# Kernel tuning notes

Hardware: AMD Instinct MI355X
Metric: run time of the kernel (lower is better)

The kernel has to match this reference:

```python
import jax, jax.numpy as jnp
import numpy as np


def setup_inputs() -> dict:
    key = jax.random.key(0)
    k1, k2 = jax.random.split(key)
    B, Lc, Lm, D = 8, 2048, 2048, 128
    context = jax.random.normal(k1, (B, Lc, D), dtype=jnp.float32)
    main = jax.random.normal(k2, (B, Lm, D), dtype=jnp.float32)
    return {"context": context, "main": main}


def reference(context, main):
    # weights[b,c,m] = sum_d context[b,c,d] * main[b,m,d]   (Keras dot axes=[2,2])
    weights = jnp.einsum("bcd,bmd->bcm", context, main)
    # K.softmax default axis=-1: normalize over the main-length axis m
    weights = jax.nn.softmax(weights, axis=-1)
    # dot([weights, context], axes=1): contract axis 1 (c) of both -> (B, Lm, D)
    weighted = jnp.einsum("bcm,bcd->bmd", weights, context)
    return main - weighted
```

## Files before the change

kernel.cpp:

```cpp
#include <hip/hip_runtime.h>


#define BATCH 8
#define L_SEQ 2048
#define DD 128
#define SHIFT 40.0f
#define LDA 136
#define TLD 136

typedef __attribute__((ext_vector_type(8))) short bf16x8;
typedef __attribute__((ext_vector_type(4))) float f32x4;
typedef __attribute__((ext_vector_type(16))) float f32x16;
typedef __attribute__((ext_vector_type(4))) unsigned int uint4v;

__device__ __forceinline__ short f2bf(float f) {
    unsigned u = __builtin_bit_cast(unsigned, f);
    return (short)((u + 0x8000u) >> 16);
}

template <int NT>
__device__ __forceinline__ void stage_tile(short* __restrict__ dst,
                                           const float* __restrict__ src,
                                           int nelts, int t) {
    for (int base = 0; base < nelts; base += NT * 8) {
        int flat = base + t * 8;
        const float4* p = (const float4*)(src + flat);
        float4 v0 = p[0];
        float4 v1 = p[1];
        bf16x8 s;
        s[0] = f2bf(v0.x); s[1] = f2bf(v0.y); s[2] = f2bf(v0.z); s[3] = f2bf(v0.w);
        s[4] = f2bf(v1.x); s[5] = f2bf(v1.y); s[6] = f2bf(v1.z); s[7] = f2bf(v1.w);
        int row = flat >> 7;
        int col = flat & 127;
        *(bf16x8*)&dst[row * LDA + col] = s;
    }
}

__global__ __launch_bounds__(256) void zero_kernel(float* __restrict__ p, int n) {
    int i = blockIdx.x * 256 + threadIdx.x;
    if (i < n) p[i] = 0.0f;
}


__global__ __launch_bounds__(256) void convert_kernel(const float* __restrict__ ctx,
                                                      const float* __restrict__ mn,
                                                      short* __restrict__ Cf,
                                                      short* __restrict__ Mf,
                                                      short* __restrict__ Ctf) {
    __shared__ short Ts[32 * TLD];

    int bid = blockIdx.x;
    int tsel = bid & 1;
    int b = (bid >> 1) & 7;
    int rg = bid >> 4;
    int t = threadIdx.x;

    const float* src = (tsel ? mn : ctx) + ((size_t)(b * L_SEQ + rg * 32)) * DD;

    #pragma unroll
    for (int i = 0; i < 2; ++i) {
        int flat = i * 2048 + t * 8;
        int r = flat >> 7;
        int d = flat & 127;
        const float4* p = (const float4*)(src + flat);
        float4 v0 = p[0];
        float4 v1 = p[1];
        bf16x8 s;
        s[0] = f2bf(v0.x); s[1] = f2bf(v0.y); s[2] = f2bf(v0.z); s[3] = f2bf(v0.w);
        s[4] = f2bf(v1.x); s[5] = f2bf(v1.y); s[6] = f2bf(v1.z); s[7] = f2bf(v1.w);
        *(bf16x8*)&Ts[r * TLD + d] = s;
    }
    __syncthreads();

    if (tsel == 0) {
        int cs = rg >> 2;
        int ch = rg & 3;
        size_t cfb = (size_t)(((b * 16 + cs) * 4 + ch) * 8) * 512;
        #pragma unroll
        for (int i = 0; i < 2; ++i) {
            int slot = i * 256 + t;
            int ks = slot >> 6;
            int l2 = slot & 63;
            int la = l2 & 31;
            int hi = l2 >> 5;
            bf16x8 v = *(const bf16x8*)&Ts[la * TLD + (ks * 2 + hi) * 8];
            *(bf16x8*)&Cf[cfb + (size_t)ks * 512 + l2 * 8] = v;
        }
        size_t ctb = (size_t)((((b * 16 + cs) * 4 + ch) * 4) * 2) * 512;
        #pragma unroll
        for (int i = 0; i < 2; ++i) {
            int slot = i * 256 + t;
            int recl = slot >> 6;
            int l2 = slot & 63;
            int dg = recl >> 1;
            int ks2 = recl & 1;
            int la = l2 & 31;
            int hi = l2 >> 5;
            int d = dg * 32 + la;
            int c0 = (ks2 * 2 + hi) * 8;
            bf16x8 v;
            #pragma unroll
            for (int j = 0; j < 8; ++j) v[j] = Ts[(c0 + j) * TLD + d];
            *(bf16x8*)&Ctf[ctb + (size_t)recl * 512 + l2 * 8] = v;
        }
    } else {
        size_t mfb = (size_t)((b * 64 + rg) * 8) * 512;
        #pragma unroll
        for (int i = 0; i < 2; ++i) {
            int slot = i * 256 + t;
            int ks = slot >> 6;
            int l2 = slot & 63;
            int la = l2 & 31;
            int hi = l2 >> 5;
            bf16x8 v = *(const bf16x8*)&Ts[la * TLD + (ks * 2 + hi) * 8];
            *(bf16x8*)&Mf[mfb + (size_t)ks * 512 + l2 * 8] = v;
        }
    }
}

__global__ __launch_bounds__(512) void stats_kernel(const short* __restrict__ Cf,
                                                    const short* __restrict__ Mf,
                                                    float* __restrict__ invLg) {
    __shared__ float red[8][2][32];

    int bid = blockIdx.x;
    int b = bid & 7;
    int ct2 = bid >> 3;
    int t = threadIdx.x;
    int w = t >> 6;
    int l = t & 63;
    int la = l & 31;

    bf16x8 cf[2][8];
    #pragma unroll
    for (int j = 0; j < 2; ++j) {
        int ct = ct2 * 2 + j;
        const short* cfp = Cf + (size_t)(((b * 16 + (ct >> 2)) * 4 + (ct & 3)) * 8) * 512 + l * 8;
        #pragma unroll
        for (int ks = 0; ks < 8; ++ks)
            cf[j][ks] = *(const bf16x8*)&cfp[(size_t)ks * 512];
    }

    float lacc0 = 0.0f, lacc1 = 0.0f;
    for (int i = 0; i < 8; ++i) {
        int mw = w * 8 + i;
        const short* mfp = Mf + (size_t)((b * 64 + mw) * 8) * 512 + l * 8;
        f32x16 s0, s1;
        #pragma unroll
        for (int r = 0; r < 16; ++r) { s0[r] = 0.0f; s1[r] = 0.0f; }
        #pragma unroll
        for (int ks = 0; ks < 8; ++ks) {
            bf16x8 av = *(const bf16x8*)&mfp[(size_t)ks * 512];
            s0 = __builtin_amdgcn_mfma_f32_32x32x16_bf16(av, cf[0][ks], s0, 0, 0, 0);
            s1 = __builtin_amdgcn_mfma_f32_32x32x16_bf16(av, cf[1][ks], s1, 0, 0, 0);
        }
        #pragma unroll
        for (int r = 0; r < 16; ++r) {
            lacc0 += __expf(s0[r] - SHIFT);
            lacc1 += __expf(s1[r] - SHIFT);
        }
    }

    lacc0 += __shfl_xor(lacc0, 32);
    lacc1 += __shfl_xor(lacc1, 32);
    if (l < 32) { red[w][0][la] = lacc0; red[w][1][la] = lacc1; }
    __syncthreads();
    if (t < 64) {
        int j = t >> 5;
        int c = t & 31;
        float L = 0.0f;
        #pragma unroll
        for (int ww = 0; ww < 8; ++ww) L += red[ww][j][c];
        invLg[(size_t)b * L_SEQ + ct2 * 64 + j * 32 + c] = 1.0f / L;
    }
}

__global__ __launch_bounds__(256, 2) void attend_fused(const short* __restrict__ Cf,
                                                       const short* __restrict__ Mf,
                                                       const short* __restrict__ Ctf,
                                                       const float* __restrict__ invLg,
                                                       const float* __restrict__ mn,
                                                       float* __restrict__ out) {
    __shared__ float red[4][4096];

    int bid = blockIdx.x;
    int b = bid & 7;
    int mtile = bid >> 3;
    int t = threadIdx.x;
    int w = t >> 6;
    int l = t & 63;
    int la = l & 31;
    int hi = l >> 5;
    int ch = w;

    bf16x8 mf[8];
    {
        const short* mfp = Mf + (size_t)((b * 64 + mtile) * 8) * 512 + l * 8;
        #pragma unroll
        for (int ks = 0; ks < 8; ++ks)
            mf[ks] = *(const bf16x8*)&mfp[(size_t)ks * 512];
    }

    f32x16 o[4];
    #pragma unroll
    for (int dg = 0; dg < 4; ++dg)
        #pragma unroll
        for (int r = 0; r < 16; ++r) o[dg][r] = 0.0f;

    const float* ilbase = invLg + (size_t)b * L_SEQ + ch * 32 + hi * 4;

    for (int cs = 0; cs < 16; ++cs) {
        const short* cfp = Cf + (size_t)(((b * 16 + cs) * 4 + ch) * 8) * 512 + l * 8;
        const short* tfp = Ctf + (size_t)((((b * 16 + cs) * 4 + ch) * 4) * 2) * 512 + l * 8;

        bf16x8 tv[4][2];
        #pragma unroll
        for (int dg = 0; dg < 4; ++dg)
            #pragma unroll
            for (int ks2 = 0; ks2 < 2; ++ks2)
                tv[dg][ks2] = *(const bf16x8*)&tfp[(size_t)(dg * 2 + ks2) * 512];

        f32x4 ilv[4];
        #pragma unroll
        for (int q = 0; q < 4; ++q)
            ilv[q] = *(const f32x4*)&ilbase[cs * 128 + q * 8];

        f32x16 s;
        #pragma unroll
        for (int r = 0; r < 16; ++r) s[r] = 0.0f;
        #pragma unroll
        for (int ks = 0; ks < 8; ++ks) {
            bf16x8 av = *(const bf16x8*)&cfp[(size_t)ks * 512];
            s = __builtin_amdgcn_mfma_f32_32x32x16_bf16(av, mf[ks], s, 0, 0, 0);
        }

        unsigned u[4][2];
        #pragma unroll
        for (int q = 0; q < 4; ++q)
            #pragma unroll
            for (int jj = 0; jj < 2; ++jj) {
                float e0 = __expf(s[q * 4 + jj * 2]     - SHIFT) * ilv[q][jj * 2];
                float e1 = __expf(s[q * 4 + jj * 2 + 1] - SHIFT) * ilv[q][jj * 2 + 1];
                u[q][jj] = ((unsigned)(unsigned short)f2bf(e1) << 16)
                         |  (unsigned)(unsigned short)f2bf(e0);
            }

        bf16x8 pa[2];
        #pragma unroll
        for (int ks2 = 0; ks2 < 2; ++ks2) {
            unsigned a0 = u[2 * ks2][0],     a1 = u[2 * ks2][1];
            unsigned b0 = u[2 * ks2 + 1][0], b1 = u[2 * ks2 + 1][1];
            unsigned a0p = (unsigned)__shfl_xor((int)a0, 32);
            unsigned a1p = (unsigned)__shfl_xor((int)a1, 32);
            unsigned b0p = (unsigned)__shfl_xor((int)b0, 32);
            unsigned b1p = (unsigned)__shfl_xor((int)b1, 32);
            uint4v pw;
            pw.x = hi ? b0p : a0;
            pw.y = hi ? b1p : a1;
            pw.z = hi ? b0  : a0p;
            pw.w = hi ? b1  : a1p;
            pa[ks2] = __builtin_bit_cast(bf16x8, pw);
        }

        #pragma unroll
        for (int dg = 0; dg < 4; ++dg)
            #pragma unroll
            for (int ks2 = 0; ks2 < 2; ++ks2)
                o[dg] = __builtin_amdgcn_mfma_f32_32x32x16_bf16(tv[dg][ks2], pa[ks2], o[dg], 0, 0, 0);
    }

    {
        float* base = red[w];
        #pragma unroll
        for (int dg = 0; dg < 4; ++dg)
            #pragma unroll
            for (int r = 0; r < 16; ++r) {
                int d = dg * 32 + (r & 3) + 8 * (r >> 2) + 4 * hi;
                base[d * 32 + la] = o[dg][r];
            }
    }
    __syncthreads();

    {
        int m  = t & 31;
        int dq = t >> 5;
        size_t gbase = ((size_t)(b * L_SEQ + mtile * 32 + m)) * DD + dq * 16;
        #pragma unroll
        for (int jq = 0; jq < 4; ++jq) {
            f32x4 v;
            #pragma unroll
            for (int e = 0; e < 4; ++e) {
                int idx = (dq * 16 + jq * 4 + e) * 32 + m;
                v[e] = red[0][idx] + red[1][idx] + red[2][idx] + red[3][idx];
            }
            f32x4 mv = *(const f32x4*)&mn[gbase + jq * 4];
            f32x4 ov;
            ov[0] = mv[0] - v[0]; ov[1] = mv[1] - v[1];
            ov[2] = mv[2] - v[2]; ov[3] = mv[3] - v[3];
            *(f32x4*)&out[gbase + jq * 4] = ov;
        }
    }
}


__global__ __launch_bounds__(256, 4) void stats_fb(const float* __restrict__ ctx,
                                                   const float* __restrict__ mn,
                                                   float* __restrict__ Lg) {
    __shared__ short Cs[64 * LDA];
    __shared__ short Ms[64 * LDA];

    int bid = blockIdx.x;
    int mc = bid & 3;
    int ct = (bid >> 2) & 31;
    int b  = bid >> 7;
    int t = threadIdx.x;
    int w = t >> 6;
    int l = t & 63;
    int a15 = l & 15;
    int q = l >> 4;

    stage_tile<256>(Cs, ctx + ((size_t)b * L_SEQ + ct * 64) * DD, 64 * DD, t);

    float ls[4] = {0.f, 0.f, 0.f, 0.f};
    for (int mt = 0; mt < 8; ++mt) {
        __syncthreads();
        int m0 = (mc * 8 + mt) * 64;
        stage_tile<256>(Ms, mn + ((size_t)b * L_SEQ + m0) * DD, 64 * DD, t);
        __syncthreads();

        f32x4 acc[4] = {{0.f,0.f,0.f,0.f},{0.f,0.f,0.f,0.f},{0.f,0.f,0.f,0.f},{0.f,0.f,0.f,0.f}};
        #pragma unroll
        for (int ks = 0; ks < 4; ++ks) {
            int k0 = ks * 32 + q * 8;
            bf16x8 a = *(const bf16x8*)&Cs[(w * 16 + a15) * LDA + k0];
            #pragma unroll
            for (int g = 0; g < 4; ++g) {
                bf16x8 bb = *(const bf16x8*)&Ms[(g * 16 + a15) * LDA + k0];
                acc[g] = __builtin_amdgcn_mfma_f32_16x16x32_bf16(a, bb, acc[g], 0, 0, 0);
            }
        }
        #pragma unroll
        for (int g = 0; g < 4; ++g)
            #pragma unroll
            for (int r = 0; r < 4; ++r)
                ls[r] += __expf(acc[g][r] - SHIFT);
    }

    #pragma unroll
    for (int r = 0; r < 4; ++r) {
        float v = ls[r];
        v += __shfl_xor(v, 1);
        v += __shfl_xor(v, 2);
        v += __shfl_xor(v, 4);
        v += __shfl_xor(v, 8);
        ls[r] = v;
    }
    if (a15 == 0) {
        int c = ct * 64 + w * 16 + q * 4;
        #pragma unroll
        for (int r = 0; r < 4; ++r)
            atomicAdd(&Lg[(size_t)b * L_SEQ + c + r], ls[r]);
    }
}

__global__ __launch_bounds__(1024, 4) void attend_fb(const float* __restrict__ ctx,
                                                     const float* __restrict__ mn,
                                                     const float* __restrict__ Lg,
                                                     float* __restrict__ out) {
    __shared__ short Mt[64 * LDA];
    __shared__ short Cs[128 * LDA];
    __shared__ short Ct[128 * LDA];
    __shared__ short Ps[64 * LDA];
    __shared__ float invLs[128];

    int bid = blockIdx.x;
    int mtile = bid & 31;
    int b = bid >> 5;
    int m0 = mtile * 64;
    int t = threadIdx.x;
    int w = t >> 6;
    int l = t & 63;
    int a15 = l & 15;
    int q = l >> 4;
    int mg = w & 3;
    int pg = w >> 2;

    stage_tile<1024>(Mt, mn + ((size_t)b * L_SEQ + m0) * DD, 64 * DD, t);

    f32x4 oacc[2] = {{0.f,0.f,0.f,0.f},{0.f,0.f,0.f,0.f}};

    for (int cs = 0; cs < 16; ++cs) {
        int c0 = cs * 128;
        __syncthreads();
        stage_tile<1024>(Cs, ctx + ((size_t)b * L_SEQ + c0) * DD, 128 * DD, t);
        if (t < 128) invLs[t] = 1.0f / Lg[(size_t)b * L_SEQ + c0 + t];
        __syncthreads();

        {
            int cc = t & 127;
            int d0 = (t >> 7) * 16;
            #pragma unroll
            for (int hh = 0; hh < 2; ++hh) {
                bf16x8 v = *(const bf16x8*)&Cs[cc * LDA + d0 + hh * 8];
                #pragma unroll
                for (int j = 0; j < 8; ++j)
                    Ct[(d0 + hh * 8 + j) * LDA + cc] = v[j];
            }
        }

        f32x4 sacc[2] = {{0.f,0.f,0.f,0.f},{0.f,0.f,0.f,0.f}};
        #pragma unroll
        for (int ks = 0; ks < 4; ++ks) {
            int k0 = ks * 32 + q * 8;
            bf16x8 a = *(const bf16x8*)&Mt[(mg * 16 + a15) * LDA + k0];
            #pragma unroll
            for (int g = 0; g < 2; ++g) {
                bf16x8 bb = *(const bf16x8*)&Cs[((pg * 2 + g) * 16 + a15) * LDA + k0];
                sacc[g] = __builtin_amdgcn_mfma_f32_16x16x32_bf16(a, bb, sacc[g], 0, 0, 0);
            }
        }
        #pragma unroll
        for (int g = 0; g < 2; ++g) {
            int cl = (pg * 2 + g) * 16 + a15;
            float il = invLs[cl];
            #pragma unroll
            for (int r = 0; r < 4; ++r) {
                float p = __expf(sacc[g][r] - SHIFT) * il;
                Ps[(mg * 16 + q * 4 + r) * LDA + cl] = f2bf(p);
            }
        }
        __syncthreads();

        #pragma unroll
        for (int ks = 0; ks < 4; ++ks) {
            int k0 = ks * 32 + q * 8;
            bf16x8 a = *(const bf16x8*)&Ps[(mg * 16 + a15) * LDA + k0];
            #pragma unroll
            for (int g = 0; g < 2; ++g) {
                bf16x8 bb = *(const bf16x8*)&Ct[((pg * 2 + g) * 16 + a15) * LDA + k0];
                oacc[g] = __builtin_amdgcn_mfma_f32_16x16x32_bf16(a, bb, oacc[g], 0, 0, 0);
            }
        }
    }

    #pragma unroll
    for (int g = 0; g < 2; ++g) {
        int dl = (pg * 2 + g) * 16 + a15;
        #pragma unroll
        for (int r = 0; r < 4; ++r) {
            int ml = mg * 16 + q * 4 + r;
            size_t idx = ((size_t)b * L_SEQ + m0 + ml) * DD + dl;
            out[idx] = mn[idx] - oacc[g][r];
        }
    }
}


extern "C" void kernel_launch(void* const* d_in, const int* in_sizes, int n_in,
                              void* d_out, int out_size, void* d_ws, size_t ws_size,
                              hipStream_t stream) {
    const float* ctx = (const float*)d_in[0];
    const float* mn  = (const float*)d_in[1];
    float* out = (float*)d_out;

    const size_t LG_BYTES = (size_t)BATCH * L_SEQ * sizeof(float);
    const size_t BF_BYTES = (size_t)BATCH * L_SEQ * DD * sizeof(short);
    const size_t NEED = LG_BYTES + 3 * BF_BYTES;

    float* Lg = (float*)d_ws;

    if (ws_size >= NEED) {
        short* Cf  = (short*)((char*)d_ws + LG_BYTES);
        short* Mf  = (short*)((char*)d_ws + LG_BYTES + BF_BYTES);
        short* Ctf = (short*)((char*)d_ws + LG_BYTES + 2 * BF_BYTES);
        convert_kernel<<<1024, 256, 0, stream>>>(ctx, mn, Cf, Mf, Ctf);
        stats_kernel<<<256, 512, 0, stream>>>(Cf, Mf, Lg);
        attend_fused<<<512, 256, 0, stream>>>(Cf, Mf, Ctf, Lg, mn, out);
    } else {
        int nL = BATCH * L_SEQ;
        zero_kernel<<<(nL + 255) / 256, 256, 0, stream>>>(Lg, nL);
        stats_fb<<<BATCH * 32 * 4, 256, 0, stream>>>(ctx, mn, Lg);
        attend_fb<<<BATCH * 32, 1024, 0, stream>>>(ctx, mn, Lg, out);
    }
}
```

Baseline: 113.8 us.

## Split stats kernel over m halves with 4 context tiles per block and atomic row sums

The stats kernel now gives each block four 32-row context tiles and half of the main sequence, in place of two tiles and the full sequence. That doubles reuse of each loaded main fragment across MFMAs and shortens each block's serial loop. Partial row sums are combined with atomicAdd into a buffer that the convert kernel zeroes, and the attend kernel takes the reciprocal at load time. The cost is extra register pressure from 32 held context fragments, atomic traffic, and a reciprocal per load in the attend loop.

```diff
diff --git a/kernel.cpp b/kernel.cpp
--- a/kernel.cpp
+++ b/kernel.cpp
@@ -46,7 +46,8 @@
                                                       const float* __restrict__ mn,
                                                       short* __restrict__ Cf,
                                                       short* __restrict__ Mf,
-                                                      short* __restrict__ Ctf) {
+                                                      short* __restrict__ Ctf,
+                                                      float* __restrict__ Lg) {
     __shared__ short Ts[32 * TLD];
 
     int bid = blockIdx.x;
@@ -54,6 +55,11 @@
     int b = (bid >> 1) & 7;
     int rg = bid >> 4;
     int t = threadIdx.x;
+
+    {
+        int tid = bid * 256 + t;
+        if (tid < BATCH * L_SEQ) Lg[tid] = 0.0f;
+    }
 
     const float* src = (tsel ? mn : ctx) + ((size_t)(b * L_SEQ + rg * 32)) * DD;
 
@@ -120,65 +126,74 @@
 
 __global__ __launch_bounds__(512) void stats_kernel(const short* __restrict__ Cf,
                                                     const short* __restrict__ Mf,
-                                                    float* __restrict__ invLg) {
-    __shared__ float red[8][2][32];
+                                                    float* __restrict__ Lg) {
+    __shared__ float red[8][4][32];
 
     int bid = blockIdx.x;
     int b = bid & 7;
-    int ct2 = bid >> 3;
+    int r2 = bid >> 3;
+    int ct4 = r2 & 15;
+    int ms = r2 >> 4;
     int t = threadIdx.x;
     int w = t >> 6;
     int l = t & 63;
     int la = l & 31;
 
-    bf16x8 cf[2][8];
+    bf16x8 cf[4][8];
     #pragma unroll
-    for (int j = 0; j < 2; ++j) {
-        int ct = ct2 * 2 + j;
-        const short* cfp = Cf + (size_t)(((b * 16 + (ct >> 2)) * 4 + (ct & 3)) * 8) * 512 + l * 8;
+    for (int j = 0; j < 4; ++j) {
+        const short* cfp = Cf + (size_t)(((b * 16 + ct4) * 4 + j) * 8) * 512 + l * 8;
         #pragma unroll
         for (int ks = 0; ks < 8; ++ks)
             cf[j][ks] = *(const bf16x8*)&cfp[(size_t)ks * 512];
     }
 
-    float lacc0 = 0.0f, lacc1 = 0.0f;
-    for (int i = 0; i < 8; ++i) {
-        int mw = w * 8 + i;
+    float lacc[4] = {0.f, 0.f, 0.f, 0.f};
+    for (int i = 0; i < 4; ++i) {
+        int mw = ms * 32 + w * 4 + i;
         const short* mfp = Mf + (size_t)((b * 64 + mw) * 8) * 512 + l * 8;
-        f32x16 s0, s1;
-        #pragma unroll
-        for (int r = 0; r < 16; ++r) { s0[r] = 0.0f; s1[r] = 0.0f; }
+        f32x16 s0, s1, s2, s3;
+        #pragma unroll
+        for (int r = 0; r < 16; ++r) { s0[r] = 0.f; s1[r] = 0.f; s2[r] = 0.f; s3[r] = 0.f; }
         #pragma unroll
         for (int ks = 0; ks < 8; ++ks) {
             bf16x8 av = *(const bf16x8*)&mfp[(size_t)ks * 512];
             s0 = __builtin_amdgcn_mfma_f32_32x32x16_bf16(av, cf[0][ks], s0, 0, 0, 0);
             s1 = __builtin_amdgcn_mfma_f32_32x32x16_bf16(av, cf[1][ks], s1, 0, 0, 0);
+            s2 = __builtin_amdgcn_mfma_f32_32x32x16_bf16(av, cf[2][ks], s2, 0, 0, 0);
+            s3 = __builtin_amdgcn_mfma_f32_32x32x16_bf16(av, cf[3][ks], s3, 0, 0, 0);
         }
         #pragma unroll
         for (int r = 0; r < 16; ++r) {
-            lacc0 += __expf(s0[r] - SHIFT);
-            lacc1 += __expf(s1[r] - SHIFT);
-        }
-    }
-
-    lacc0 += __shfl_xor(lacc0, 32);
-    lacc1 += __shfl_xor(lacc1, 32);
-    if (l < 32) { red[w][0][la] = lacc0; red[w][1][la] = lacc1; }
+            lacc[0] += __expf(s0[r] - SHIFT);
+            lacc[1] += __expf(s1[r] - SHIFT);
+            lacc[2] += __expf(s2[r] - SHIFT);
+            lacc[3] += __expf(s3[r] - SHIFT);
+        }
+    }
+
+    #pragma unroll
+    for (int j = 0; j < 4; ++j)
+        lacc[j] += __shfl_xor(lacc[j], 32);
+    if (l < 32) {
+        #pragma unroll
+        for (int j = 0; j < 4; ++j) red[w][j][la] = lacc[j];
+    }
     __syncthreads();
-    if (t < 64) {
+    if (t < 128) {
         int j = t >> 5;
         int c = t & 31;
         float L = 0.0f;
         #pragma unroll
         for (int ww = 0; ww < 8; ++ww) L += red[ww][j][c];
-        invLg[(size_t)b * L_SEQ + ct2 * 64 + j * 32 + c] = 1.0f / L;
+        atomicAdd(&Lg[(size_t)b * L_SEQ + ct4 * 128 + j * 32 + c], L);
     }
 }
 
 __global__ __launch_bounds__(256, 2) void attend_fused(const short* __restrict__ Cf,
                                                        const short* __restrict__ Mf,
                                                        const short* __restrict__ Ctf,
-                                                       const float* __restrict__ invLg,
+                                                       const float* __restrict__ Lg,
                                                        const float* __restrict__ mn,
                                                        float* __restrict__ out) {
     __shared__ float red[4][4096];
@@ -207,7 +222,7 @@
         #pragma unroll
         for (int r = 0; r < 16; ++r) o[dg][r] = 0.0f;
 
-    const float* ilbase = invLg + (size_t)b * L_SEQ + ch * 32 + hi * 4;
+    const float* ilbase = Lg + (size_t)b * L_SEQ + ch * 32 + hi * 4;
 
     for (int cs = 0; cs < 16; ++cs) {
         const short* cfp = Cf + (size_t)(((b * 16 + cs) * 4 + ch) * 8) * 512 + l * 8;
@@ -222,8 +237,12 @@
 
         f32x4 ilv[4];
         #pragma unroll
-        for (int q = 0; q < 4; ++q)
-            ilv[q] = *(const f32x4*)&ilbase[cs * 128 + q * 8];
+        for (int q = 0; q < 4; ++q) {
+            f32x4 lv = *(const f32x4*)&ilbase[cs * 128 + q * 8];
+            #pragma unroll
+            for (int e = 0; e < 4; ++e)
+                ilv[q][e] = __builtin_amdgcn_rcpf(lv[e]);
+        }
 
         f32x16 s;
         #pragma unroll
@@ -473,7 +492,7 @@
         short* Cf  = (short*)((char*)d_ws + LG_BYTES);
         short* Mf  = (short*)((char*)d_ws + LG_BYTES + BF_BYTES);
         short* Ctf = (short*)((char*)d_ws + LG_BYTES + 2 * BF_BYTES);
-        convert_kernel<<<1024, 256, 0, stream>>>(ctx, mn, Cf, Mf, Ctf);
+        convert_kernel<<<1024, 256, 0, stream>>>(ctx, mn, Cf, Mf, Ctf, Lg);
         stats_kernel<<<256, 512, 0, stream>>>(Cf, Mf, Lg);
         attend_fused<<<512, 256, 0, stream>>>(Cf, Mf, Ctf, Lg, mn, out);
     } else {
```

Result: no change. 112.7 us (-1.0%).
